# Performance work log

Hardware: AMD Instinct MI355X
Metric: run time of the kernel (lower is better)

The kernel has to match this reference:

```python
import jax, jax.numpy as jnp
import numpy as np

NUM_HEADS = 12

def setup_inputs() -> dict:
    key = jax.random.key(0)
    ks = jax.random.split(key, 6)
    B, N, C, T = 1, 4096, 768, 16
    return {
        "x": jax.random.normal(ks[0], (B, N, C), dtype=jnp.float32),
        "templates": jax.random.normal(ks[1], (T, 3 * C, C), dtype=jnp.float32) * 0.02,
        "coeffs": jax.random.normal(ks[2], (2, T, 1), dtype=jnp.float32),
        "qkv_bias": jnp.zeros((3 * C,), dtype=jnp.float32),
        "proj_w": jax.random.normal(ks[3], (C, C), dtype=jnp.float32) * 0.02,
        "proj_b": jnp.zeros((C,), dtype=jnp.float32),
    }

def reference(x, templates, coeffs, qkv_bias, proj_w, proj_b):
    B, N, C = x.shape
    H = NUM_HEADS
    hd = C // H
    scale = hd ** -0.5
    # template bank: each of num_cf coefficient sets builds a (3C, C) weight; average them
    num_cf = coeffs.shape[0]
    qkv_w = jnp.einsum('kt,toi->oi', coeffs[:, :, 0], templates) / num_cf  # (3C, C)
    qkv = x @ qkv_w.T + qkv_bias                                          # (B, N, 3C)
    qkv = qkv.reshape(B, N, 3, H, hd).transpose(2, 0, 3, 1, 4)            # (3, B, H, N, hd)
    q, k, v = qkv[0], qkv[1], qkv[2]
    attn = jax.nn.softmax(jnp.einsum('bhnd,bhmd->bhnm', q, k) * scale, axis=-1)
    out = jnp.einsum('bhnm,bhmd->bhnd', attn, v)                          # (B, H, N, hd)
    out = out.transpose(0, 2, 1, 3).reshape(B, N, C)
    return out @ proj_w.T + proj_b
```

## Files before the change

### kernel.cpp

```cpp
#include <hip/hip_runtime.h>
#include <stdint.h>

#define N_SEQ 4096
#define C_DIM 768
#define HEADS 12
#define HD    64
#define OI    (2304*768)

typedef __attribute__((ext_vector_type(8))) short short8;
typedef __attribute__((ext_vector_type(4))) float f32x4;
typedef __attribute__((ext_vector_type(16))) float f32x16;

__device__ __forceinline__ short f2bf(float f) {
  union { float f; unsigned u; } v; v.f = f;
  unsigned r = v.u + 0x7FFF + ((v.u >> 16) & 1);
  return (short)(r >> 16);
}

__global__ __launch_bounds__(256) void prep_qkvw(const float* __restrict__ tmpl,
                                                 const float* __restrict__ coeffs,
                                                 short* __restrict__ w_bf) {
  __shared__ float c[16];
  if (threadIdx.x < 16)
    c[threadIdx.x] = 0.5f * (coeffs[threadIdx.x] + coeffs[16 + threadIdx.x]);
  __syncthreads();
  int idx = blockIdx.x * 256 + threadIdx.x;
  int base = idx * 4;
  if (base >= OI) return;
  float ax = 0.f, ay = 0.f, az = 0.f, aw = 0.f;
#pragma unroll
  for (int t = 0; t < 16; ++t) {
    float4 v = *(const float4*)(tmpl + (size_t)t * OI + base);
    float ct = c[t];
    ax = fmaf(ct, v.x, ax); ay = fmaf(ct, v.y, ay);
    az = fmaf(ct, v.z, az); aw = fmaf(ct, v.w, aw);
  }
  short4 o = make_short4(f2bf(ax), f2bf(ay), f2bf(az), f2bf(aw));
  *(short4*)(w_bf + base) = o;
}

__global__ __launch_bounds__(256) void cvt_bf16(const float* __restrict__ src,
                                                short* __restrict__ dst, int n4) {
  int i = blockIdx.x * 256 + threadIdx.x;
  if (i >= n4) return;
  float4 v = ((const float4*)src)[i];
  ((short4*)dst)[i] = make_short4(f2bf(v.x), f2bf(v.y), f2bf(v.z), f2bf(v.w));
}

#define GST 40
#define QSCALE 0.1803368801111204f
__global__ __launch_bounds__(256) void gemm_qkv(const short* __restrict__ A,
                                                const short* __restrict__ B,
                                                const float* __restrict__ bias,
                                                short* __restrict__ qkv_out) {
  __shared__ short As[128 * GST];
  __shared__ short Bs[128 * GST];
  int tid = threadIdx.x;
  int wave = tid >> 6, lane = tid & 63, g = lane >> 4, l15 = lane & 15;
  int wm = (wave >> 1) * 64, wn = (wave & 1) * 64;
  size_t mblk = (size_t)blockIdx.x * 128;
  size_t nblk = (size_t)blockIdx.y * 128;

  f32x4 acc[4][4];
#pragma unroll
  for (int mi = 0; mi < 4; ++mi)
#pragma unroll
    for (int ni = 0; ni < 4; ++ni)
#pragma unroll
      for (int r = 0; r < 4; ++r) acc[mi][ni][r] = 0.f;

  int row0 = tid >> 2;
  int c8   = (tid & 3) * 8;

  for (int k0 = 0; k0 < 768; k0 += 32) {
    short8 a0 = *(const short8*)(A + (mblk + row0) * 768 + k0 + c8);
    short8 a1 = *(const short8*)(A + (mblk + row0 + 64) * 768 + k0 + c8);
    short8 b0 = *(const short8*)(B + (nblk + row0) * 768 + k0 + c8);
    short8 b1 = *(const short8*)(B + (nblk + row0 + 64) * 768 + k0 + c8);
    __syncthreads();
    *(short8*)(As + row0 * GST + c8) = a0;
    *(short8*)(As + (row0 + 64) * GST + c8) = a1;
    *(short8*)(Bs + row0 * GST + c8) = b0;
    *(short8*)(Bs + (row0 + 64) * GST + c8) = b1;
    __syncthreads();
    short8 af[4], bfr[4];
#pragma unroll
    for (int mi = 0; mi < 4; ++mi)
      af[mi] = *(const short8*)(As + (wm + mi * 16 + l15) * GST + g * 8);
#pragma unroll
    for (int ni = 0; ni < 4; ++ni)
      bfr[ni] = *(const short8*)(Bs + (wn + ni * 16 + l15) * GST + g * 8);
#pragma unroll
    for (int mi = 0; mi < 4; ++mi)
#pragma unroll
      for (int ni = 0; ni < 4; ++ni)
        acc[mi][ni] = __builtin_amdgcn_mfma_f32_16x16x32_bf16(af[mi], bfr[ni], acc[mi][ni], 0, 0, 0);
  }

#pragma unroll
  for (int ni = 0; ni < 4; ++ni) {
    int col = (int)nblk + wn + ni * 16 + l15;
    int which = col / 768;
    int rem = col - which * 768;
    int h = rem >> 6, d = rem & 63;
    float bcol = bias[col];
    if (which == 2) {
      short* vbase = qkv_out + (size_t)2 * HEADS * N_SEQ * HD
                   + ((size_t)h * HD + d) * N_SEQ;
#pragma unroll
      for (int mi = 0; mi < 4; ++mi) {
        int rowb = (int)mblk + wm + mi * 16 + g * 4;
        short4 o;
        o.x = f2bf(acc[mi][ni][0] + bcol);
        o.y = f2bf(acc[mi][ni][1] + bcol);
        o.z = f2bf(acc[mi][ni][2] + bcol);
        o.w = f2bf(acc[mi][ni][3] + bcol);
        *(short4*)(vbase + rowb) = o;
      }
    } else {
      float sc = (which == 0) ? QSCALE : 1.0f;
      short* dst = qkv_out + ((size_t)which * HEADS + h) * N_SEQ * HD + d;
#pragma unroll
      for (int mi = 0; mi < 4; ++mi) {
        int rowb = (int)mblk + wm + mi * 16 + g * 4;
#pragma unroll
        for (int r = 0; r < 4; ++r)
          dst[(size_t)(rowb + r) * HD] = f2bf((acc[mi][ni][r] + bcol) * sc);
      }
    }
  }
}

__global__ __launch_bounds__(256) void gemm_proj(const short* __restrict__ A,
                                                 const short* __restrict__ B,
                                                 const float* __restrict__ bias,
                                                 float* __restrict__ C) {
  __shared__ short As[64 * GST];
  __shared__ short Bs[64 * GST];
  int tid = threadIdx.x;
  int wave = tid >> 6, lane = tid & 63, g = lane >> 4, l15 = lane & 15;
  int wm = (wave >> 1) * 32, wn = (wave & 1) * 32;
  size_t mblk = (size_t)blockIdx.x * 64;
  size_t nblk = (size_t)blockIdx.y * 64;

  f32x4 acc[2][2];
#pragma unroll
  for (int mi = 0; mi < 2; ++mi)
#pragma unroll
    for (int ni = 0; ni < 2; ++ni)
#pragma unroll
      for (int r = 0; r < 4; ++r) acc[mi][ni][r] = 0.f;

  int row0 = tid >> 2;
  int c8   = (tid & 3) * 8;

  for (int k0 = 0; k0 < 768; k0 += 32) {
    short8 a0 = *(const short8*)(A + (mblk + row0) * 768 + k0 + c8);
    short8 b0 = *(const short8*)(B + (nblk + row0) * 768 + k0 + c8);
    __syncthreads();
    *(short8*)(As + row0 * GST + c8) = a0;
    *(short8*)(Bs + row0 * GST + c8) = b0;
    __syncthreads();
    short8 af[2], bfr[2];
#pragma unroll
    for (int mi = 0; mi < 2; ++mi)
      af[mi] = *(const short8*)(As + (wm + mi * 16 + l15) * GST + g * 8);
#pragma unroll
    for (int ni = 0; ni < 2; ++ni)
      bfr[ni] = *(const short8*)(Bs + (wn + ni * 16 + l15) * GST + g * 8);
#pragma unroll
    for (int mi = 0; mi < 2; ++mi)
#pragma unroll
      for (int ni = 0; ni < 2; ++ni)
        acc[mi][ni] = __builtin_amdgcn_mfma_f32_16x16x32_bf16(af[mi], bfr[ni], acc[mi][ni], 0, 0, 0);
  }

#pragma unroll
  for (int ni = 0; ni < 2; ++ni) {
    int col = (int)nblk + wn + ni * 16 + l15;
    float bcol = bias[col];
#pragma unroll
    for (int mi = 0; mi < 2; ++mi) {
      int rowb = (int)mblk + wm + mi * 16 + g * 4;
#pragma unroll
      for (int r = 0; r < 4; ++r)
        C[(size_t)(rowb + r) * 768 + col] = acc[mi][ni][r] + bcol;
    }
  }
}

#define PST 68
__global__ __launch_bounds__(256, 2) void attn_fa(const short* __restrict__ qkv_buf,
                                                  float* __restrict__ op0,
                                                  float* __restrict__ op1,
                                                  float* __restrict__ lp) {
  __shared__ short Ks[2][64 * PST];
  __shared__ short Vt[2][64 * PST];
  int bid = blockIdx.x;
  int j = (bid & 7) * 96 + (bid >> 3);
  int h = j >> 6;
  int rj = j & 63;
  int half = rj >> 5;
  int qt = rj & 31;
  int tid = threadIdx.x, wave = tid >> 6, lane = tid & 63;
  int q5 = lane & 31, h5 = lane >> 5;
  int qb = qt * 128 + wave * 32;
  int kvb = half * 2048;
  const short* qh  = qkv_buf + (size_t)(0 * HEADS + h) * N_SEQ * HD;
  const short* kh  = qkv_buf + (size_t)(1 * HEADS + h) * N_SEQ * HD;
  const short* vth = qkv_buf + (size_t)2 * HEADS * N_SEQ * HD + (size_t)h * HD * N_SEQ;

  short8 qf[4];
#pragma unroll
  for (int c = 0; c < 4; ++c)
    qf[c] = *(const short8*)(qh + (size_t)(qb + q5) * HD + c * 16 + h5 * 8);

  f32x16 o_acc[2];
#pragma unroll
  for (int dt = 0; dt < 2; ++dt)
#pragma unroll
    for (int r = 0; r < 16; ++r) o_acc[dt][r] = 0.f;
  float l_r = 0.f;

  int srow = tid >> 2;
  int sq   = (tid & 3) * 16;

  short8 kr[2], vr[2];
#pragma unroll
  for (int i = 0; i < 2; ++i) {
    kr[i] = *(const short8*)(kh + (size_t)(kvb + srow) * HD + sq + 8 * i);
    vr[i] = *(const short8*)(vth + (size_t)srow * N_SEQ + kvb + sq + 8 * i);
  }
#pragma unroll
  for (int i = 0; i < 2; ++i) {
    *(short8*)(&Ks[0][srow * PST + sq + 8 * i]) = kr[i];
    *(short8*)(&Vt[0][srow * PST + sq + 8 * i]) = vr[i];
  }
#pragma unroll
  for (int i = 0; i < 2; ++i) {
    kr[i] = *(const short8*)(kh + (size_t)(kvb + 64 + srow) * HD + sq + 8 * i);
    vr[i] = *(const short8*)(vth + (size_t)srow * N_SEQ + kvb + 64 + sq + 8 * i);
  }

  for (int it = 0; it < 32; ++it) {
    int cur = it & 1;
    __syncthreads();

    if (it + 1 < 32) {
#pragma unroll
      for (int i = 0; i < 2; ++i) {
        *(short8*)(&Ks[cur ^ 1][srow * PST + sq + 8 * i]) = kr[i];
        *(short8*)(&Vt[cur ^ 1][srow * PST + sq + 8 * i]) = vr[i];
      }
      if (it + 2 < 32) {
        int t2 = kvb + (it + 2) * 64;
#pragma unroll
        for (int i = 0; i < 2; ++i) {
          kr[i] = *(const short8*)(kh + (size_t)(t2 + srow) * HD + sq + 8 * i);
          vr[i] = *(const short8*)(vth + (size_t)srow * N_SEQ + t2 + sq + 8 * i);
        }
      }
    }

    f32x16 st[2];
#pragma unroll
    for (int kt = 0; kt < 2; ++kt)
#pragma unroll
      for (int r = 0; r < 16; ++r) st[kt][r] = 0.f;
#pragma unroll
    for (int c = 0; c < 4; ++c)
#pragma unroll
      for (int kt = 0; kt < 2; ++kt) {
        short8 kf = *(const short8*)(&Ks[cur][(kt * 32 + q5) * PST + c * 16 + h5 * 8]);
        st[kt] = __builtin_amdgcn_mfma_f32_32x32x16_bf16(kf, qf[c], st[kt], 0, 0, 0);
      }

    short8 pf[4];
#pragma unroll
    for (int kt = 0; kt < 2; ++kt)
#pragma unroll
      for (int cm = 0; cm < 2; ++cm) {
        float p0 = __builtin_amdgcn_exp2f(st[kt][cm * 8 + 0]);
        float p1 = __builtin_amdgcn_exp2f(st[kt][cm * 8 + 1]);
        float p2 = __builtin_amdgcn_exp2f(st[kt][cm * 8 + 2]);
        float p3 = __builtin_amdgcn_exp2f(st[kt][cm * 8 + 3]);
        float p4 = __builtin_amdgcn_exp2f(st[kt][cm * 8 + 4]);
        float p5 = __builtin_amdgcn_exp2f(st[kt][cm * 8 + 5]);
        float p6 = __builtin_amdgcn_exp2f(st[kt][cm * 8 + 6]);
        float p7 = __builtin_amdgcn_exp2f(st[kt][cm * 8 + 7]);
        l_r += ((p0 + p1) + (p2 + p3)) + ((p4 + p5) + (p6 + p7));
        unsigned X1, Y1, X2, Y2;
        asm("v_cvt_pk_bf16_f32 %0, %1, %2" : "=v"(X1) : "v"(p0), "v"(p1));
        asm("v_cvt_pk_bf16_f32 %0, %1, %2" : "=v"(Y1) : "v"(p4), "v"(p5));
        asm("v_cvt_pk_bf16_f32 %0, %1, %2" : "=v"(X2) : "v"(p2), "v"(p3));
        asm("v_cvt_pk_bf16_f32 %0, %1, %2" : "=v"(Y2) : "v"(p6), "v"(p7));
        asm("v_permlane32_swap_b32 %0, %1" : "+v"(X1), "+v"(Y1));
        asm("v_permlane32_swap_b32 %0, %1" : "+v"(X2), "+v"(Y2));
        union { unsigned u[4]; short8 s; } w;
        w.u[0] = X1; w.u[1] = X2; w.u[2] = Y1; w.u[3] = Y2;
        pf[kt * 2 + cm] = w.s;
      }

#pragma unroll
    for (int c = 0; c < 4; ++c)
#pragma unroll
      for (int dt = 0; dt < 2; ++dt) {
        short8 vf = *(const short8*)(&Vt[cur][(dt * 32 + q5) * PST + c * 16 + h5 * 8]);
        o_acc[dt] = __builtin_amdgcn_mfma_f32_32x32x16_bf16(pf[c], vf, o_acc[dt], 0, 0, 0);
      }
  }

  float* op = half ? op1 : op0;
  float l = l_r + __shfl_xor(l_r, 32);
#pragma unroll
  for (int cc = 0; cc < 4; ++cc)
#pragma unroll
    for (int rr = 0; rr < 4; ++rr) {
      int qloc = rr + 8 * cc + 4 * h5;
      size_t base = ((size_t)h * N_SEQ + qb + qloc) * HD;
#pragma unroll
      for (int dt = 0; dt < 2; ++dt)
        op[base + dt * 32 + q5] = o_acc[dt][cc * 4 + rr];
    }
  if (h5 == 0)
    lp[((size_t)half * HEADS + h) * N_SEQ + qb + q5] = l;
}

__global__ __launch_bounds__(256) void attn_reduce(const float* __restrict__ op0,
                                                   const float* __restrict__ op1,
                                                   const float* __restrict__ lp,
                                                   short* __restrict__ out_bf) {
  int idx = blockIdx.x * 256 + threadIdx.x;
  int d4 = idx & 15;
  int n  = (idx >> 4) & 4095;
  int h  = idx >> 16;
  size_t o = ((size_t)h * N_SEQ + n) * HD + d4 * 4;
  float4 a = *(const float4*)(op0 + o);
  float4 b = *(const float4*)(op1 + o);
  float l = lp[(size_t)h * N_SEQ + n] + lp[((size_t)HEADS + h) * N_SEQ + n];
  float inv = 1.0f / l;
  short4 s = make_short4(f2bf((a.x + b.x) * inv), f2bf((a.y + b.y) * inv),
                         f2bf((a.z + b.z) * inv), f2bf((a.w + b.w) * inv));
  *(short4*)(out_bf + (size_t)n * C_DIM + h * HD + d4 * 4) = s;
}

extern "C" void kernel_launch(void* const* d_in, const int* in_sizes, int n_in,
                              void* d_out, int out_size, void* d_ws, size_t ws_size,
                              hipStream_t stream) {
  const float* x        = (const float*)d_in[0];
  const float* tmpl     = (const float*)d_in[1];
  const float* coeffs   = (const float*)d_in[2];
  const float* qkv_bias = (const float*)d_in[3];
  const float* proj_w   = (const float*)d_in[4];
  const float* proj_b   = (const float*)d_in[5];
  float* out = (float*)d_out;
  char* ws = (char*)d_ws;

  short* w_bf    = (short*)(ws);
  short* x_bf    = (short*)(ws + 3538944);
  short* pw_bf   = (short*)(ws + 9830400);
  short* qkvb    = (short*)(ws + 11010048);
  short* attn_bf = (short*)(ws + 29884416);
  float* opart1  = (float*)(ws + 36175872);
  float* lpart   = (float*)(ws + 48758784);
  float* opart0  = out;

  prep_qkvw<<<1728, 256, 0, stream>>>(tmpl, coeffs, w_bf);
  cvt_bf16<<<3072, 256, 0, stream>>>(x, x_bf, 786432);
  cvt_bf16<<<576, 256, 0, stream>>>(proj_w, pw_bf, 147456);

  dim3 g1(32, 18);
  gemm_qkv<<<g1, 256, 0, stream>>>(x_bf, w_bf, qkv_bias, qkvb);

  attn_fa<<<768, 256, 0, stream>>>(qkvb, opart0, opart1, lpart);
  attn_reduce<<<3072, 256, 0, stream>>>(opart0, opart1, lpart, attn_bf);

  dim3 g2(64, 12);
  gemm_proj<<<g2, 256, 0, stream>>>(attn_bf, pw_bf, proj_b, out);
}
```

Measured before the change: 306.2 us.

## Double-buffer LDS tiles with register prefetch in QKV and projection GEMMs

Both GEMM kernels now keep two LDS buffers and prefetch the tile two steps ahead into registers, so the kernel needs one barrier per K step instead of two. The next tile's LDS store and the following global load overlap with the MFMA work on the current buffer. The cost is double the LDS footprint and more live registers, which may lower occupancy. The attention kernel probably dominates the runtime, so the GEMMs are only part of the total.

```diff
diff --git a/kernel.cpp b/kernel.cpp
--- a/kernel.cpp
+++ b/kernel.cpp
@@ -53,8 +53,8 @@
                                                 const short* __restrict__ B,
                                                 const float* __restrict__ bias,
                                                 short* __restrict__ qkv_out) {
-  __shared__ short As[128 * GST];
-  __shared__ short Bs[128 * GST];
+  __shared__ short As[2][128 * GST];
+  __shared__ short Bs[2][128 * GST];
   int tid = threadIdx.x;
   int wave = tid >> 6, lane = tid & 63, g = lane >> 4, l15 = lane & 15;
   int wm = (wave >> 1) * 64, wn = (wave & 1) * 64;
@@ -72,24 +72,44 @@
   int row0 = tid >> 2;
   int c8   = (tid & 3) * 8;
 
-  for (int k0 = 0; k0 < 768; k0 += 32) {
-    short8 a0 = *(const short8*)(A + (mblk + row0) * 768 + k0 + c8);
-    short8 a1 = *(const short8*)(A + (mblk + row0 + 64) * 768 + k0 + c8);
-    short8 b0 = *(const short8*)(B + (nblk + row0) * 768 + k0 + c8);
-    short8 b1 = *(const short8*)(B + (nblk + row0 + 64) * 768 + k0 + c8);
+  short8 a0 = *(const short8*)(A + (mblk + row0) * 768 + c8);
+  short8 a1 = *(const short8*)(A + (mblk + row0 + 64) * 768 + c8);
+  short8 b0 = *(const short8*)(B + (nblk + row0) * 768 + c8);
+  short8 b1 = *(const short8*)(B + (nblk + row0 + 64) * 768 + c8);
+  *(short8*)(&As[0][row0 * GST + c8]) = a0;
+  *(short8*)(&As[0][(row0 + 64) * GST + c8]) = a1;
+  *(short8*)(&Bs[0][row0 * GST + c8]) = b0;
+  *(short8*)(&Bs[0][(row0 + 64) * GST + c8]) = b1;
+  a0 = *(const short8*)(A + (mblk + row0) * 768 + 32 + c8);
+  a1 = *(const short8*)(A + (mblk + row0 + 64) * 768 + 32 + c8);
+  b0 = *(const short8*)(B + (nblk + row0) * 768 + 32 + c8);
+  b1 = *(const short8*)(B + (nblk + row0 + 64) * 768 + 32 + c8);
+
+  for (int it = 0; it < 24; ++it) {
+    int cur = it & 1;
     __syncthreads();
-    *(short8*)(As + row0 * GST + c8) = a0;
-    *(short8*)(As + (row0 + 64) * GST + c8) = a1;
-    *(short8*)(Bs + row0 * GST + c8) = b0;
-    *(short8*)(Bs + (row0 + 64) * GST + c8) = b1;
-    __syncthreads();
+
+    if (it + 1 < 24) {
+      *(short8*)(&As[cur ^ 1][row0 * GST + c8]) = a0;
+      *(short8*)(&As[cur ^ 1][(row0 + 64) * GST + c8]) = a1;
+      *(short8*)(&Bs[cur ^ 1][row0 * GST + c8]) = b0;
+      *(short8*)(&Bs[cur ^ 1][(row0 + 64) * GST + c8]) = b1;
+      if (it + 2 < 24) {
+        int k0 = (it + 2) * 32;
+        a0 = *(const short8*)(A + (mblk + row0) * 768 + k0 + c8);
+        a1 = *(const short8*)(A + (mblk + row0 + 64) * 768 + k0 + c8);
+        b0 = *(const short8*)(B + (nblk + row0) * 768 + k0 + c8);
+        b1 = *(const short8*)(B + (nblk + row0 + 64) * 768 + k0 + c8);
+      }
+    }
+
     short8 af[4], bfr[4];
 #pragma unroll
     for (int mi = 0; mi < 4; ++mi)
-      af[mi] = *(const short8*)(As + (wm + mi * 16 + l15) * GST + g * 8);
+      af[mi] = *(const short8*)(&As[cur][(wm + mi * 16 + l15) * GST + g * 8]);
 #pragma unroll
     for (int ni = 0; ni < 4; ++ni)
-      bfr[ni] = *(const short8*)(Bs + (wn + ni * 16 + l15) * GST + g * 8);
+      bfr[ni] = *(const short8*)(&Bs[cur][(wn + ni * 16 + l15) * GST + g * 8]);
 #pragma unroll
     for (int mi = 0; mi < 4; ++mi)
 #pragma unroll
@@ -135,8 +155,8 @@
                                                  const short* __restrict__ B,
                                                  const float* __restrict__ bias,
                                                  float* __restrict__ C) {
-  __shared__ short As[64 * GST];
-  __shared__ short Bs[64 * GST];
+  __shared__ short As[2][64 * GST];
+  __shared__ short Bs[2][64 * GST];
   int tid = threadIdx.x;
   int wave = tid >> 6, lane = tid & 63, g = lane >> 4, l15 = lane & 15;
   int wm = (wave >> 1) * 32, wn = (wave & 1) * 32;
@@ -154,20 +174,34 @@
   int row0 = tid >> 2;
   int c8   = (tid & 3) * 8;
 
-  for (int k0 = 0; k0 < 768; k0 += 32) {
-    short8 a0 = *(const short8*)(A + (mblk + row0) * 768 + k0 + c8);
-    short8 b0 = *(const short8*)(B + (nblk + row0) * 768 + k0 + c8);
+  short8 a0 = *(const short8*)(A + (mblk + row0) * 768 + c8);
+  short8 b0 = *(const short8*)(B + (nblk + row0) * 768 + c8);
+  *(short8*)(&As[0][row0 * GST + c8]) = a0;
+  *(short8*)(&Bs[0][row0 * GST + c8]) = b0;
+  a0 = *(const short8*)(A + (mblk + row0) * 768 + 32 + c8);
+  b0 = *(const short8*)(B + (nblk + row0) * 768 + 32 + c8);
+
+  for (int it = 0; it < 24; ++it) {
+    int cur = it & 1;
     __syncthreads();
-    *(short8*)(As + row0 * GST + c8) = a0;
-    *(short8*)(Bs + row0 * GST + c8) = b0;
-    __syncthreads();
+
+    if (it + 1 < 24) {
+      *(short8*)(&As[cur ^ 1][row0 * GST + c8]) = a0;
+      *(short8*)(&Bs[cur ^ 1][row0 * GST + c8]) = b0;
+      if (it + 2 < 24) {
+        int k0 = (it + 2) * 32;
+        a0 = *(const short8*)(A + (mblk + row0) * 768 + k0 + c8);
+        b0 = *(const short8*)(B + (nblk + row0) * 768 + k0 + c8);
+      }
+    }
+
     short8 af[2], bfr[2];
 #pragma unroll
     for (int mi = 0; mi < 2; ++mi)
-      af[mi] = *(const short8*)(As + (wm + mi * 16 + l15) * GST + g * 8);
+      af[mi] = *(const short8*)(&As[cur][(wm + mi * 16 + l15) * GST + g * 8]);
 #pragma unroll
     for (int ni = 0; ni < 2; ++ni)
-      bfr[ni] = *(const short8*)(Bs + (wn + ni * 16 + l15) * GST + g * 8);
+      bfr[ni] = *(const short8*)(&Bs[cur][(wn + ni * 16 + l15) * GST + g * 8]);
 #pragma unroll
     for (int mi = 0; mi < 2; ++mi)
 #pragma unroll
```

Result: faster. 297.4 us (-2.9%).
